# Kernel tuning notes

Hardware: AMD Instinct MI355X
Metric: run time of the kernel (lower is better)

## Reference

```python
import jax, jax.numpy as jnp
import numpy as np

N, M, D = 62, 512, 256  # parts, batch samples (P*K = 64*8), hidden dim
K_PER_ID = 8
MARGIN = 0.2


def setup_inputs() -> dict:
    key = jax.random.key(0)
    k1, = jax.random.split(key, 1)
    feature = jax.random.normal(k1, (N, M, D), dtype=jnp.float32)
    # P*K structured labels (uniform class sizes are REQUIRED by the original
    # masked_select(...).view(n, m, -1) reshape): 64 ids, 8 samples each,
    # identical label layout for every part row n.
    row = jnp.arange(M, dtype=jnp.int64) // K_PER_ID  # [M]
    label = jnp.tile(row[None, :], (N, 1))            # [N, M]
    return {"feature": feature, "label": label}


def _safe_sqrt(x):
    # sqrt(relu(x)) with a zero (finite) gradient at x <= 0, matching the
    # forward values of torch.sqrt(F.relu(x)) exactly.
    pos = x > 0
    return jnp.where(pos, jnp.sqrt(jnp.where(pos, x, 1.0)), 0.0)


def reference(feature, label):
    # feature: [n, m, d], label: [n, m]
    sq = jnp.sum(feature * feature, axis=2)                       # [n, m]
    gram = jnp.einsum('nmd,nkd->nmk', feature, feature)           # [n, m, m]
    d2 = sq[:, :, None] + sq[:, None, :] - 2.0 * gram             # [n, m, m]
    dist = _safe_sqrt(jnp.maximum(d2, 0.0))                       # [n, m, m]

    dist_mean = jnp.mean(dist, axis=(1, 2))                       # [n]

    pos_mask = label[:, :, None] == label[:, None, :]             # [n, m, m]
    # hard positive: max dist over same-label columns (incl. self)
    hard_hp = jnp.max(jnp.where(pos_mask, dist, -jnp.inf), axis=2)   # [n, m]
    # hard negative: min dist over different-label columns
    hard_hn = jnp.min(jnp.where(pos_mask, jnp.inf, dist), axis=2)    # [n, m]

    hard_loss = jax.nn.relu(MARGIN + hard_hp - hard_hn)           # [n, m]
    hard_loss_mean = jnp.mean(hard_loss, axis=1)                  # [n]
    return hard_loss_mean, dist_mean
```

## Files before the change

kernel.cpp:

```cpp
#include <hip/hip_runtime.h>

#define N_PARTS 62
#define M_SAMP  512
#define D_DIM   256
#define MARGIN  0.2f

typedef unsigned short ushort_t;
typedef __attribute__((ext_vector_type(8))) short bf16x8;
typedef __attribute__((ext_vector_type(4))) float f32x4;

typedef const __attribute__((address_space(1))) unsigned gu32;
typedef __attribute__((address_space(3))) unsigned lu32;

__device__ __forceinline__ ushort_t bf16_rne(float f) {
    unsigned u = __float_as_uint(f);
    unsigned r = u + 0x7fffu + ((u >> 16) & 1u);
    return (ushort_t)(r >> 16);
}

__device__ __forceinline__ float bf16_val(float f) {
    return __uint_as_float((unsigned)bf16_rne(f) << 16);
}

__device__ __forceinline__ bf16x8 cvt_frag(f32x4 a0, f32x4 a1) {
    union { bf16x8 v; unsigned u[4]; } r;
    r.u[0] = (unsigned)bf16_rne(a0.x) | ((unsigned)bf16_rne(a0.y) << 16);
    r.u[1] = (unsigned)bf16_rne(a0.z) | ((unsigned)bf16_rne(a0.w) << 16);
    r.u[2] = (unsigned)bf16_rne(a1.x) | ((unsigned)bf16_rne(a1.y) << 16);
    r.u[3] = (unsigned)bf16_rne(a1.z) | ((unsigned)bf16_rne(a1.w) << 16);
    return r.v;
}

__global__ void zero_out_kernel(float* __restrict__ out) {
    if (threadIdx.x < 2 * N_PARTS) out[threadIdx.x] = 0.0f;
}

__global__ __launch_bounds__(512)
__attribute__((amdgpu_waves_per_eu(2, 4)))
void fused_kernel(const float* __restrict__ feat, float* __restrict__ out) {
    const int id = blockIdx.x;
    const int n  = id & 63;
    const int ct = id >> 6;
    if (n >= N_PARTS) return;
    const int tid  = threadIdx.x;
    const int wave = tid >> 6, lane = tid & 63;

    __shared__ float tile[2][512 * 32];
    __shared__ float sqA[M_SAMP];
    __shared__ float mrg[8][64][3];

    const float* fpart = feat + (size_t)n * (M_SAMP * D_DIM);

    const int srow = lane >> 3;
    const int scol = (lane & 7) ^ srow;
    const float* gbase = fpart + (size_t)srow * D_DIM + (size_t)scol * 4;

    #pragma unroll
    for (int j = 0; j < 8; ++j) {
        const int s = wave + 8 * j;
        __builtin_amdgcn_global_load_lds(
            (gu32*)(gbase + (size_t)s * 8 * D_DIM),
            (lu32*)(uintptr_t)&tile[0][s * 256], 16, 0, 0);
    }
    __syncthreads();

    const int fr  = lane & 15;
    const int q   = lane >> 4;
    const int sl1 = (2 * q) ^ (fr & 7);
    const int sl2 = (2 * q + 1) ^ (fr & 7);
    const int aoff = (wave * 64 + fr) * 32;
    const int boff = (ct * 64 + fr) * 32;
    const int soff = tid * 32;
    const int sx   = tid & 7;

    f32x4 acc[4][4] = {};
    float sqp = 0.f;

    #pragma unroll
    for (int c = 0; c < 8; ++c) {
        const float* tb = tile[c & 1];
        if (c < 7) {
            float* tn = tile[(c + 1) & 1];
            #pragma unroll
            for (int j = 0; j < 8; ++j) {
                const int s = wave + 8 * j;
                __builtin_amdgcn_global_load_lds(
                    (gu32*)(gbase + (size_t)s * 8 * D_DIM + (c + 1) * 32),
                    (lu32*)(uintptr_t)&tn[s * 256], 16, 0, 0);
            }
        }
        #pragma unroll
        for (int s = 0; s < 8; ++s) {
            const f32x4 v = *(const f32x4*)&tb[soff + ((s ^ sx) << 2)];
            const float a = bf16_val(v.x), b = bf16_val(v.y),
                        e = bf16_val(v.z), d = bf16_val(v.w);
            sqp += a * a + b * b + e * e + d * d;
        }
        bf16x8 af[4];
        #pragma unroll
        for (int mi = 0; mi < 4; ++mi)
            af[mi] = cvt_frag(*(const f32x4*)&tb[aoff + mi * 512 + sl1 * 4],
                              *(const f32x4*)&tb[aoff + mi * 512 + sl2 * 4]);
        #pragma unroll
        for (int ni = 0; ni < 4; ++ni) {
            const bf16x8 bfv = cvt_frag(*(const f32x4*)&tb[boff + ni * 512 + sl1 * 4],
                                        *(const f32x4*)&tb[boff + ni * 512 + sl2 * 4]);
            #pragma unroll
            for (int mi = 0; mi < 4; ++mi)
                acc[mi][ni] = __builtin_amdgcn_mfma_f32_16x16x32_bf16(
                    af[mi], bfv, acc[mi][ni], 0, 0, 0);
        }
        __syncthreads();
    }

    sqA[tid] = sqp;
    __syncthreads();

    float sqr[4][4];
    #pragma unroll
    for (int mi = 0; mi < 4; ++mi)
        #pragma unroll
        for (int p = 0; p < 4; ++p)
            sqr[mi][p] = sqA[wave * 64 + mi * 16 + (lane >> 4) * 4 + p];

    #pragma unroll
    for (int ni = 0; ni < 4; ++ni) {
        const int C = ct * 64 + ni * 16 + (lane & 15);
        const float sc = sqA[C];
        const int Cg = C >> 3;
        float ds = 0.f, hp = 0.f, hn = 1e30f;
        #pragma unroll
        for (int mi = 0; mi < 4; ++mi) {
            #pragma unroll
            for (int p = 0; p < 4; ++p) {
                const int R = wave * 64 + mi * 16 + (lane >> 4) * 4 + p;
                const float d2 = sqr[mi][p] + sc - 2.f * acc[mi][ni][p];
                const float d  = __builtin_amdgcn_sqrtf(fmaxf(d2, 0.f));
                ds += d;
                if ((R >> 3) == Cg) hp = fmaxf(hp, d);
                else                hn = fminf(hn, d);
            }
        }
        #pragma unroll
        for (int off = 16; off < 64; off <<= 1) {
            ds += __shfl_xor(ds, off);
            hp = fmaxf(hp, __shfl_xor(hp, off));
            hn = fminf(hn, __shfl_xor(hn, off));
        }
        if (lane < 16) {
            mrg[wave][ni * 16 + lane][0] = hp;
            mrg[wave][ni * 16 + lane][1] = hn;
            mrg[wave][ni * 16 + lane][2] = ds;
        }
    }
    __syncthreads();
    if (tid < 64) {
        float hp = 0.f, hn = 1e30f, bd = 0.f;
        #pragma unroll
        for (int w = 0; w < 8; ++w) {
            hp = fmaxf(hp, mrg[w][tid][0]);
            hn = fminf(hn, mrg[w][tid][1]);
            bd += mrg[w][tid][2];
        }
        float bl = fmaxf(MARGIN + hp - hn, 0.f);
        #pragma unroll
        for (int off = 32; off > 0; off >>= 1) {
            bl += __shfl_xor(bl, off);
            bd += __shfl_xor(bd, off);
        }
        if (tid == 0) {
            atomicAdd(&out[n],           bl * (1.0f / 512.0f));
            atomicAdd(&out[N_PARTS + n], bd * (1.0f / (512.0f * 512.0f)));
        }
    }
}

extern "C" void kernel_launch(void* const* d_in, const int* in_sizes, int n_in,
                              void* d_out, int out_size, void* d_ws, size_t ws_size,
                              hipStream_t stream) {
    const float* feat = (const float*)d_in[0];
    float* out = (float*)d_out;
    (void)d_ws; (void)ws_size;

    zero_out_kernel<<<dim3(1), 128, 0, stream>>>(out);
    fused_kernel<<<dim3(8 * 64), 512, 0, stream>>>(feat, out);
}
```

Baseline: 104.3 us.

## Convert features to bf16 once during staging into padded LDS tile

Measured after the change: 146.0 us. 1.4x slower.

```diff
diff --git a/kernel.cpp b/kernel.cpp
--- a/kernel.cpp
+++ b/kernel.cpp
@@ -4,31 +4,16 @@
 #define M_SAMP  512
 #define D_DIM   256
 #define MARGIN  0.2f
+#define RSTRIDE 40
 
 typedef unsigned short ushort_t;
 typedef __attribute__((ext_vector_type(8))) short bf16x8;
 typedef __attribute__((ext_vector_type(4))) float f32x4;
-
-typedef const __attribute__((address_space(1))) unsigned gu32;
-typedef __attribute__((address_space(3))) unsigned lu32;
 
 __device__ __forceinline__ ushort_t bf16_rne(float f) {
     unsigned u = __float_as_uint(f);
     unsigned r = u + 0x7fffu + ((u >> 16) & 1u);
     return (ushort_t)(r >> 16);
-}
-
-__device__ __forceinline__ float bf16_val(float f) {
-    return __uint_as_float((unsigned)bf16_rne(f) << 16);
-}
-
-__device__ __forceinline__ bf16x8 cvt_frag(f32x4 a0, f32x4 a1) {
-    union { bf16x8 v; unsigned u[4]; } r;
-    r.u[0] = (unsigned)bf16_rne(a0.x) | ((unsigned)bf16_rne(a0.y) << 16);
-    r.u[1] = (unsigned)bf16_rne(a0.z) | ((unsigned)bf16_rne(a0.w) << 16);
-    r.u[2] = (unsigned)bf16_rne(a1.x) | ((unsigned)bf16_rne(a1.y) << 16);
-    r.u[3] = (unsigned)bf16_rne(a1.z) | ((unsigned)bf16_rne(a1.w) << 16);
-    return r.v;
 }
 
 __global__ void zero_out_kernel(float* __restrict__ out) {
@@ -45,75 +30,104 @@
     const int tid  = threadIdx.x;
     const int wave = tid >> 6, lane = tid & 63;
 
-    __shared__ float tile[2][512 * 32];
+    __shared__ ushort_t tile[2][512 * RSTRIDE];
     __shared__ float sqA[M_SAMP];
     __shared__ float mrg[8][64][3];
 
-    const float* fpart = feat + (size_t)n * (M_SAMP * D_DIM);
-
-    const int srow = lane >> 3;
-    const int scol = (lane & 7) ^ srow;
-    const float* gbase = fpart + (size_t)srow * D_DIM + (size_t)scol * 4;
-
-    #pragma unroll
-    for (int j = 0; j < 8; ++j) {
-        const int s = wave + 8 * j;
-        __builtin_amdgcn_global_load_lds(
-            (gu32*)(gbase + (size_t)s * 8 * D_DIM),
-            (lu32*)(uintptr_t)&tile[0][s * 256], 16, 0, 0);
+    const int rq = tid >> 2;
+    const int sl = tid & 3;
+    const float* fb = feat + (size_t)n * (M_SAMP * D_DIM)
+                    + (size_t)rq * D_DIM + sl * 8;
+
+    f32x4 acc[4][4] = {};
+    float sqp[4] = {0.f, 0.f, 0.f, 0.f};
+
+    {
+        float4 va[4], vb[4];
+        #pragma unroll
+        for (int j = 0; j < 4; ++j) {
+            const float* p = fb + (size_t)j * 128 * D_DIM;
+            va[j] = *(const float4*)(p);
+            vb[j] = *(const float4*)(p + 4);
+        }
+        #pragma unroll
+        for (int j = 0; j < 4; ++j) {
+            const int row = j * 128 + rq;
+            union { bf16x8 v; ushort_t s[8]; } u;
+            u.s[0] = bf16_rne(va[j].x); u.s[1] = bf16_rne(va[j].y);
+            u.s[2] = bf16_rne(va[j].z); u.s[3] = bf16_rne(va[j].w);
+            u.s[4] = bf16_rne(vb[j].x); u.s[5] = bf16_rne(vb[j].y);
+            u.s[6] = bf16_rne(vb[j].z); u.s[7] = bf16_rne(vb[j].w);
+            float s = 0.f;
+            #pragma unroll
+            for (int e = 0; e < 8; ++e) {
+                const float r = __uint_as_float((unsigned)u.s[e] << 16);
+                s += r * r;
+            }
+            sqp[j] += s;
+            *(bf16x8*)&tile[0][row * RSTRIDE + sl * 8] = u.v;
+        }
     }
     __syncthreads();
 
-    const int fr  = lane & 15;
-    const int q   = lane >> 4;
-    const int sl1 = (2 * q) ^ (fr & 7);
-    const int sl2 = (2 * q + 1) ^ (fr & 7);
-    const int aoff = (wave * 64 + fr) * 32;
-    const int boff = (ct * 64 + fr) * 32;
-    const int soff = tid * 32;
-    const int sx   = tid & 7;
-
-    f32x4 acc[4][4] = {};
-    float sqp = 0.f;
+    const int fr = lane & 15, q = lane >> 4;
+    const int abase = (wave * 64 + fr) * RSTRIDE + q * 8;
+    const int bbase = (ct * 64 + fr) * RSTRIDE + q * 8;
 
     #pragma unroll
     for (int c = 0; c < 8; ++c) {
-        const float* tb = tile[c & 1];
+        float4 va[4], vb[4];
         if (c < 7) {
-            float* tn = tile[(c + 1) & 1];
-            #pragma unroll
-            for (int j = 0; j < 8; ++j) {
-                const int s = wave + 8 * j;
-                __builtin_amdgcn_global_load_lds(
-                    (gu32*)(gbase + (size_t)s * 8 * D_DIM + (c + 1) * 32),
-                    (lu32*)(uintptr_t)&tn[s * 256], 16, 0, 0);
-            }
-        }
-        #pragma unroll
-        for (int s = 0; s < 8; ++s) {
-            const f32x4 v = *(const f32x4*)&tb[soff + ((s ^ sx) << 2)];
-            const float a = bf16_val(v.x), b = bf16_val(v.y),
-                        e = bf16_val(v.z), d = bf16_val(v.w);
-            sqp += a * a + b * b + e * e + d * d;
-        }
+            #pragma unroll
+            for (int j = 0; j < 4; ++j) {
+                const float* p = fb + (size_t)j * 128 * D_DIM + (c + 1) * 32;
+                va[j] = *(const float4*)(p);
+                vb[j] = *(const float4*)(p + 4);
+            }
+        }
+        const ushort_t* tb = tile[c & 1];
         bf16x8 af[4];
         #pragma unroll
         for (int mi = 0; mi < 4; ++mi)
-            af[mi] = cvt_frag(*(const f32x4*)&tb[aoff + mi * 512 + sl1 * 4],
-                              *(const f32x4*)&tb[aoff + mi * 512 + sl2 * 4]);
+            af[mi] = *(const bf16x8*)&tb[abase + mi * 16 * RSTRIDE];
         #pragma unroll
         for (int ni = 0; ni < 4; ++ni) {
-            const bf16x8 bfv = cvt_frag(*(const f32x4*)&tb[boff + ni * 512 + sl1 * 4],
-                                        *(const f32x4*)&tb[boff + ni * 512 + sl2 * 4]);
+            const bf16x8 bfv = *(const bf16x8*)&tb[bbase + ni * 16 * RSTRIDE];
             #pragma unroll
             for (int mi = 0; mi < 4; ++mi)
                 acc[mi][ni] = __builtin_amdgcn_mfma_f32_16x16x32_bf16(
                     af[mi], bfv, acc[mi][ni], 0, 0, 0);
         }
+        if (c < 7) {
+            ushort_t* tn = tile[(c + 1) & 1];
+            #pragma unroll
+            for (int j = 0; j < 4; ++j) {
+                const int row = j * 128 + rq;
+                union { bf16x8 v; ushort_t s[8]; } u;
+                u.s[0] = bf16_rne(va[j].x); u.s[1] = bf16_rne(va[j].y);
+                u.s[2] = bf16_rne(va[j].z); u.s[3] = bf16_rne(va[j].w);
+                u.s[4] = bf16_rne(vb[j].x); u.s[5] = bf16_rne(vb[j].y);
+                u.s[6] = bf16_rne(vb[j].z); u.s[7] = bf16_rne(vb[j].w);
+                float s = 0.f;
+                #pragma unroll
+                for (int e = 0; e < 8; ++e) {
+                    const float r = __uint_as_float((unsigned)u.s[e] << 16);
+                    s += r * r;
+                }
+                sqp[j] += s;
+                *(bf16x8*)&tn[row * RSTRIDE + sl * 8] = u.v;
+            }
+        }
         __syncthreads();
     }
 
-    sqA[tid] = sqp;
+    #pragma unroll
+    for (int j = 0; j < 4; ++j) {
+        float s = sqp[j];
+        s += __shfl_xor(s, 1);
+        s += __shfl_xor(s, 2);
+        if (sl == 0) sqA[j * 128 + wave * 16 + (lane >> 2)] = s;
+    }
     __syncthreads();
 
     float sqr[4][4];
```

## Convert each fp32 chunk once to a padded bf16 LDS tile before MFMA

Applied to the files above, without the earlier changes.

Result: faster. 100.5 us (-3.6%).

```diff
diff --git a/kernel.cpp b/kernel.cpp
--- a/kernel.cpp
+++ b/kernel.cpp
@@ -4,6 +4,7 @@
 #define M_SAMP  512
 #define D_DIM   256
 #define MARGIN  0.2f
+#define RSTRIDE 40
 
 typedef unsigned short ushort_t;
 typedef __attribute__((ext_vector_type(8))) short bf16x8;
@@ -16,19 +17,6 @@
     unsigned u = __float_as_uint(f);
     unsigned r = u + 0x7fffu + ((u >> 16) & 1u);
     return (ushort_t)(r >> 16);
-}
-
-__device__ __forceinline__ float bf16_val(float f) {
-    return __uint_as_float((unsigned)bf16_rne(f) << 16);
-}
-
-__device__ __forceinline__ bf16x8 cvt_frag(f32x4 a0, f32x4 a1) {
-    union { bf16x8 v; unsigned u[4]; } r;
-    r.u[0] = (unsigned)bf16_rne(a0.x) | ((unsigned)bf16_rne(a0.y) << 16);
-    r.u[1] = (unsigned)bf16_rne(a0.z) | ((unsigned)bf16_rne(a0.w) << 16);
-    r.u[2] = (unsigned)bf16_rne(a1.x) | ((unsigned)bf16_rne(a1.y) << 16);
-    r.u[3] = (unsigned)bf16_rne(a1.z) | ((unsigned)bf16_rne(a1.w) << 16);
-    return r.v;
 }
 
 __global__ void zero_out_kernel(float* __restrict__ out) {
@@ -45,9 +33,10 @@
     const int tid  = threadIdx.x;
     const int wave = tid >> 6, lane = tid & 63;
 
-    __shared__ float tile[2][512 * 32];
-    __shared__ float sqA[M_SAMP];
-    __shared__ float mrg[8][64][3];
+    __shared__ float    f32buf[512 * 32];
+    __shared__ ushort_t bt[2][512 * RSTRIDE];
+    __shared__ float    sqA[M_SAMP];
+    __shared__ float    mrg[8][64][3];
 
     const float* fpart = feat + (size_t)n * (M_SAMP * D_DIM);
 
@@ -60,57 +49,72 @@
         const int s = wave + 8 * j;
         __builtin_amdgcn_global_load_lds(
             (gu32*)(gbase + (size_t)s * 8 * D_DIM),
-            (lu32*)(uintptr_t)&tile[0][s * 256], 16, 0, 0);
+            (lu32*)(uintptr_t)&f32buf[s * 256], 16, 0, 0);
     }
     __syncthreads();
 
-    const int fr  = lane & 15;
-    const int q   = lane >> 4;
-    const int sl1 = (2 * q) ^ (fr & 7);
-    const int sl2 = (2 * q + 1) ^ (fr & 7);
-    const int aoff = (wave * 64 + fr) * 32;
-    const int boff = (ct * 64 + fr) * 32;
-    const int soff = tid * 32;
-    const int sx   = tid & 7;
+    const int sx = tid & 7;
+    float sqp = 0.f;
+
+#define CONVERT_CHUNK(DST)                                                   \
+    {                                                                        \
+        ushort_t* dp = (DST) + tid * RSTRIDE;                                \
+        _Pragma("unroll")                                                    \
+        for (int i = 0; i < 8; i += 2) {                                     \
+            const f32x4 v0 = *(const f32x4*)&f32buf[tid * 32 + ((i ^ sx) << 2)];       \
+            const f32x4 v1 = *(const f32x4*)&f32buf[tid * 32 + (((i + 1) ^ sx) << 2)]; \
+            union { bf16x8 v; ushort_t s[8]; } u;                            \
+            u.s[0] = bf16_rne(v0.x); u.s[1] = bf16_rne(v0.y);                \
+            u.s[2] = bf16_rne(v0.z); u.s[3] = bf16_rne(v0.w);                \
+            u.s[4] = bf16_rne(v1.x); u.s[5] = bf16_rne(v1.y);                \
+            u.s[6] = bf16_rne(v1.z); u.s[7] = bf16_rne(v1.w);                \
+            _Pragma("unroll")                                                \
+            for (int e = 0; e < 8; ++e) {                                    \
+                const float r = __uint_as_float((unsigned)u.s[e] << 16);     \
+                sqp += r * r;                                                \
+            }                                                                \
+            *(bf16x8*)&dp[(i >> 1) * 8] = u.v;                               \
+        }                                                                    \
+    }
+
+    CONVERT_CHUNK(bt[0]);
+    __syncthreads();
+
+    const int fr = lane & 15, q = lane >> 4;
+    const int abase = (wave * 64 + fr) * RSTRIDE + q * 8;
+    const int bbase = (ct * 64 + fr) * RSTRIDE + q * 8;
 
     f32x4 acc[4][4] = {};
-    float sqp = 0.f;
 
     #pragma unroll
     for (int c = 0; c < 8; ++c) {
-        const float* tb = tile[c & 1];
         if (c < 7) {
-            float* tn = tile[(c + 1) & 1];
             #pragma unroll
             for (int j = 0; j < 8; ++j) {
                 const int s = wave + 8 * j;
                 __builtin_amdgcn_global_load_lds(
                     (gu32*)(gbase + (size_t)s * 8 * D_DIM + (c + 1) * 32),
-                    (lu32*)(uintptr_t)&tn[s * 256], 16, 0, 0);
+                    (lu32*)(uintptr_t)&f32buf[s * 256], 16, 0, 0);
             }
         }
-        #pragma unroll
-        for (int s = 0; s < 8; ++s) {
-            const f32x4 v = *(const f32x4*)&tb[soff + ((s ^ sx) << 2)];
-            const float a = bf16_val(v.x), b = bf16_val(v.y),
-                        e = bf16_val(v.z), d = bf16_val(v.w);
-            sqp += a * a + b * b + e * e + d * d;
-        }
+        const ushort_t* tb = bt[c & 1];
         bf16x8 af[4];
         #pragma unroll
         for (int mi = 0; mi < 4; ++mi)
-            af[mi] = cvt_frag(*(const f32x4*)&tb[aoff + mi * 512 + sl1 * 4],
-                              *(const f32x4*)&tb[aoff + mi * 512 + sl2 * 4]);
+            af[mi] = *(const bf16x8*)&tb[abase + mi * 16 * RSTRIDE];
         #pragma unroll
         for (int ni = 0; ni < 4; ++ni) {
-            const bf16x8 bfv = cvt_frag(*(const f32x4*)&tb[boff + ni * 512 + sl1 * 4],
-                                        *(const f32x4*)&tb[boff + ni * 512 + sl2 * 4]);
+            const bf16x8 bfv = *(const bf16x8*)&tb[bbase + ni * 16 * RSTRIDE];
             #pragma unroll
             for (int mi = 0; mi < 4; ++mi)
                 acc[mi][ni] = __builtin_amdgcn_mfma_f32_16x16x32_bf16(
                     af[mi], bfv, acc[mi][ni], 0, 0, 0);
         }
         __syncthreads();
+        if (c < 7) {
+            CONVERT_CHUNK(bt[(c + 1) & 1]);
+            __syncthreads();
+        }
     }
 
     sqA[tid] = sqp;
```
